# Kernel optimization log

Measured on AMD Instinct MI355X. Metric: run time of the kernel, lower is better.

## Reference

```python
import jax, jax.numpy as jnp
import numpy as np

DT = 0.001  # forward's default dt
EPS = 1e-10


def setup_inputs() -> dict:
    key = jax.random.key(0)
    k1, k2 = jax.random.split(key)
    nt, ntr, nc = 4096, 1024, 3
    x = jax.random.normal(k1, (nt, ntr, nc), dtype=jnp.float32)
    y = jax.random.normal(k2, (nt, ntr, nc), dtype=jnp.float32)
    return {"x": x, "y": y}


def reference(x, y):
    # x, y: [nt, ntraces, nchannels]
    nt = x.shape[0]
    # autocorrelation energy per (trace, channel) column via Parseval-style FFT sum
    X = jnp.fft.fft(x, axis=0)
    Y = jnp.fft.fft(y, axis=0)
    Ex = DT * jnp.sum(jnp.abs(X) ** 2, axis=0) / nt + EPS  # [ntr, nc]
    Ey = DT * jnp.sum(jnp.abs(Y) ** 2, axis=0) / nt + EPS  # [ntr, nc]
    dots = jnp.sum(x * y, axis=0)                          # [ntr, nc]
    cc = dots / jnp.sqrt(Ex * Ey)                          # [ntr, nc]
    # original skips columns whose max |x| is exactly 0
    mask = jnp.max(jnp.abs(x), axis=0) > 0
    loss = jnp.sum(jnp.where(mask, cc, 0.0))
    return loss
```

## Files before the change

### kernel.cpp

```cpp
#include <hip/hip_runtime.h>


#define NT 4096
#define NCOL 3072
#define NCOL4 768
#define CGROUPS 12
#define TCHUNKS 64
#define WTS 16
#define BATCH 8

typedef float vfloat4 __attribute__((ext_vector_type(4)));

#define PS_STRIDE_STAT (TCHUNKS * NCOL)

__global__ __launch_bounds__(256, 3) void ncc_stage1(const float* __restrict__ x,
                                                     const float* __restrict__ y,
                                                     float* __restrict__ ws) {
    const int bx   = blockIdx.x;
    const int cg   = bx % CGROUPS;
    const int tc   = bx / CGROUPS;
    const int tid  = threadIdx.x;
    const int w    = tid >> 6;
    const int lane = tid & 63;
    const int col4 = cg * 64 + lane;

    const int tbase = tc * 64 + w * WTS;
    const vfloat4* __restrict__ x4 =
        reinterpret_cast<const vfloat4*>(x) + (size_t)tbase * NCOL4 + col4;
    const vfloat4* __restrict__ y4 =
        reinterpret_cast<const vfloat4*>(y) + (size_t)tbase * NCOL4 + col4;

    vfloat4 sx2 = {0.f, 0.f, 0.f, 0.f};
    vfloat4 sy2 = {0.f, 0.f, 0.f, 0.f};
    vfloat4 sxy = {0.f, 0.f, 0.f, 0.f};

#pragma unroll
    for (int b = 0; b < WTS / BATCH; ++b) {
        vfloat4 xv[BATCH], yv[BATCH];
#pragma unroll
        for (int i = 0; i < BATCH; ++i) {
            const int t = b * BATCH + i;
            xv[i] = x4[t * NCOL4];
            yv[i] = y4[t * NCOL4];
        }
#pragma unroll
        for (int i = 0; i < BATCH; ++i) {
            sx2 = xv[i] * xv[i] + sx2;
            sy2 = yv[i] * yv[i] + sy2;
            sxy = xv[i] * yv[i] + sxy;
        }
    }

    __shared__ vfloat4 red[3][4][64];
    red[0][w][lane] = sx2;
    red[1][w][lane] = sy2;
    red[2][w][lane] = sxy;
    __syncthreads();

    if (w < 3) {
        vfloat4 s = red[w][0][lane] + red[w][1][lane] + red[w][2][lane] + red[w][3][lane];
        vfloat4* __restrict__ ps = reinterpret_cast<vfloat4*>(ws);
        ps[(w * TCHUNKS + tc) * NCOL4 + col4] = s;
    }
}

__global__ __launch_bounds__(256) void ncc_stage2(const float* __restrict__ ws,
                                                  float* __restrict__ out) {
    const int b    = blockIdx.x;
    const int tid  = threadIdx.x;
    const int lane = tid & 63;
    const int q    = tid >> 6;
    const int j    = b * 64 + lane;

    float sx2 = 0.f, sy2 = 0.f, sxy = 0.f;
    const int c0 = q * (TCHUNKS / 4);
#pragma unroll
    for (int c = c0; c < c0 + TCHUNKS / 4; ++c) {
        sx2 += ws[0 * PS_STRIDE_STAT + c * NCOL + j];
        sy2 += ws[1 * PS_STRIDE_STAT + c * NCOL + j];
        sxy += ws[2 * PS_STRIDE_STAT + c * NCOL + j];
    }

    __shared__ float red[3][4][64];
    red[0][q][lane] = sx2;
    red[1][q][lane] = sy2;
    red[2][q][lane] = sxy;
    __syncthreads();

    if (q == 0) {
        sx2 = red[0][0][lane] + red[0][1][lane] + red[0][2][lane] + red[0][3][lane];
        sy2 = red[1][0][lane] + red[1][1][lane] + red[1][2][lane] + red[1][3][lane];
        sxy = red[2][0][lane] + red[2][1][lane] + red[2][2][lane] + red[2][3][lane];
        float ex = fmaf(0.001f, sx2, 1e-10f);
        float ey = fmaf(0.001f, sy2, 1e-10f);
        float cc = (sx2 > 0.f) ? sxy * rsqrtf(ex * ey) : 0.f;
#pragma unroll
        for (int off = 32; off > 0; off >>= 1)
            cc += __shfl_down(cc, off, 64);
        if (lane == 0)
            atomicAdd(out, cc);
    }
}

extern "C" void kernel_launch(void* const* d_in, const int* in_sizes, int n_in,
                              void* d_out, int out_size, void* d_ws, size_t ws_size,
                              hipStream_t stream) {
    const float* x = reinterpret_cast<const float*>(d_in[0]);
    const float* y = reinterpret_cast<const float*>(d_in[1]);
    float* out = reinterpret_cast<float*>(d_out);
    float* ws = reinterpret_cast<float*>(d_ws);

    ncc_stage1<<<dim3(CGROUPS * TCHUNKS), dim3(256), 0, stream>>>(x, y, ws);
    ncc_stage2<<<dim3(48), dim3(256), 0, stream>>>(ws, out);
}
```

Baseline: 115.3 us.

## Fuse both reduction stages into one cooperative kernel with grid sync

Merges the partial-sum kernel and the final reduction kernel into a single cooperative launch, using a grid-wide barrier between the phases so only the first 48 blocks do the final reduction. This removes the second kernel launch and its gap. In exchange it adds a grid sync across 768 blocks, which requires every block to be co-resident, and a cooperative launch carries its own overhead.

```diff
diff --git a/kernel.cpp b/kernel.cpp
--- a/kernel.cpp
+++ b/kernel.cpp
@@ -1,4 +1,5 @@
 #include <hip/hip_runtime.h>
+#include <hip/hip_cooperative_groups.h>
 
 
 #define NT 4096
@@ -13,16 +14,17 @@
 
 #define PS_STRIDE_STAT (TCHUNKS * NCOL)
 
-__global__ __launch_bounds__(256, 3) void ncc_stage1(const float* __restrict__ x,
-                                                     const float* __restrict__ y,
-                                                     float* __restrict__ ws) {
+__global__ __launch_bounds__(256, 3) void ncc_fused(const float* __restrict__ x,
+                                                    const float* __restrict__ y,
+                                                    float* __restrict__ ws,
+                                                    float* __restrict__ out) {
     const int bx   = blockIdx.x;
-    const int cg   = bx % CGROUPS;
+    const int cgp  = bx % CGROUPS;
     const int tc   = bx / CGROUPS;
     const int tid  = threadIdx.x;
     const int w    = tid >> 6;
     const int lane = tid & 63;
-    const int col4 = cg * 64 + lane;
+    const int col4 = cgp * 64 + lane;
 
     const int tbase = tc * 64 + w * WTS;
     const vfloat4* __restrict__ x4 =
@@ -62,43 +64,41 @@
         vfloat4* __restrict__ ps = reinterpret_cast<vfloat4*>(ws);
         ps[(w * TCHUNKS + tc) * NCOL4 + col4] = s;
     }
-}
 
-__global__ __launch_bounds__(256) void ncc_stage2(const float* __restrict__ ws,
-                                                  float* __restrict__ out) {
-    const int b    = blockIdx.x;
-    const int tid  = threadIdx.x;
-    const int lane = tid & 63;
-    const int q    = tid >> 6;
-    const int j    = b * 64 + lane;
+    cooperative_groups::this_grid().sync();
 
-    float sx2 = 0.f, sy2 = 0.f, sxy = 0.f;
-    const int c0 = q * (TCHUNKS / 4);
+    if (bx < 48) {
+        const int q = w;
+        const int j = bx * 64 + lane;
+
+        float a = 0.f, b2 = 0.f, c2 = 0.f;
+        const int c0 = q * (TCHUNKS / 4);
 #pragma unroll
-    for (int c = c0; c < c0 + TCHUNKS / 4; ++c) {
-        sx2 += ws[0 * PS_STRIDE_STAT + c * NCOL + j];
-        sy2 += ws[1 * PS_STRIDE_STAT + c * NCOL + j];
-        sxy += ws[2 * PS_STRIDE_STAT + c * NCOL + j];
-    }
+        for (int c = c0; c < c0 + TCHUNKS / 4; ++c) {
+            a  += ws[0 * PS_STRIDE_STAT + c * NCOL + j];
+            b2 += ws[1 * PS_STRIDE_STAT + c * NCOL + j];
+            c2 += ws[2 * PS_STRIDE_STAT + c * NCOL + j];
+        }
 
-    __shared__ float red[3][4][64];
-    red[0][q][lane] = sx2;
-    red[1][q][lane] = sy2;
-    red[2][q][lane] = sxy;
-    __syncthreads();
+        __shared__ float red2[3][4][64];
+        red2[0][q][lane] = a;
+        red2[1][q][lane] = b2;
+        red2[2][q][lane] = c2;
+        __syncthreads();
 
-    if (q == 0) {
-        sx2 = red[0][0][lane] + red[0][1][lane] + red[0][2][lane] + red[0][3][lane];
-        sy2 = red[1][0][lane] + red[1][1][lane] + red[1][2][lane] + red[1][3][lane];
-        sxy = red[2][0][lane] + red[2][1][lane] + red[2][2][lane] + red[2][3][lane];
-        float ex = fmaf(0.001f, sx2, 1e-10f);
-        float ey = fmaf(0.001f, sy2, 1e-10f);
-        float cc = (sx2 > 0.f) ? sxy * rsqrtf(ex * ey) : 0.f;
+        if (q == 0) {
+            float sx = red2[0][0][lane] + red2[0][1][lane] + red2[0][2][lane] + red2[0][3][lane];
+            float sy = red2[1][0][lane] + red2[1][1][lane] + red2[1][2][lane] + red2[1][3][lane];
+            float sc = red2[2][0][lane] + red2[2][1][lane] + red2[2][2][lane] + red2[2][3][lane];
+            float ex = fmaf(0.001f, sx, 1e-10f);
+            float ey = fmaf(0.001f, sy, 1e-10f);
+            float cc = (sx > 0.f) ? sc * rsqrtf(ex * ey) : 0.f;
 #pragma unroll
-        for (int off = 32; off > 0; off >>= 1)
-            cc += __shfl_down(cc, off, 64);
-        if (lane == 0)
-            atomicAdd(out, cc);
+            for (int off = 32; off > 0; off >>= 1)
+                cc += __shfl_down(cc, off, 64);
+            if (lane == 0)
+                atomicAdd(out, cc);
+        }
     }
 }
 
@@ -110,6 +110,8 @@
     float* out = reinterpret_cast<float*>(d_out);
     float* ws = reinterpret_cast<float*>(d_ws);
 
-    ncc_stage1<<<dim3(CGROUPS * TCHUNKS), dim3(256), 0, stream>>>(x, y, ws);
-    ncc_stage2<<<dim3(48), dim3(256), 0, stream>>>(ws, out);
+    void* args[] = {(void*)&x, (void*)&y, (void*)&ws, (void*)&out};
+    hipLaunchCooperativeKernel(reinterpret_cast<void*>(ncc_fused),
+                               dim3(CGROUPS * TCHUNKS), dim3(256),
+                               args, 0, stream);
 }
```

New measurement: 207.8 us. 1.8x slower.
